# Kernel tuning notes

Measured on AMD Instinct MI355X. Metric: run time of the kernel, lower is better.

Reference implementation:

```python
import jax, jax.numpy as jnp
import numpy as np
import math

ROPE_THETA = 10000.0


def apply_rope(x, positions):
    # x: [B, H, S, d_k], positions: [S]
    d_k = x.shape[-1]
    inv_freq = 1.0 / (ROPE_THETA ** (jnp.arange(0, d_k, 2, dtype=jnp.float32) / d_k))  # [d_k/2]
    angles = positions.astype(jnp.float32)[:, None] * inv_freq[None, :]  # [S, d_k/2]
    cos = jnp.cos(angles)
    sin = jnp.sin(angles)
    x1 = x[..., 0::2]
    x2 = x[..., 1::2]
    r1 = x1 * cos - x2 * sin
    r2 = x1 * sin + x2 * cos
    out = jnp.stack([r1, r2], axis=-1)  # interleave pairs back
    return out.reshape(x.shape)


def setup_inputs() -> dict:
    key = jax.random.key(0)
    k1, k2, k3 = jax.random.split(key, 3)
    B, S, D = 4, 2048, 1024
    x = jax.random.normal(k1, (B, S, D), dtype=jnp.float32)
    token_positions = jnp.arange(S, dtype=jnp.int32)
    w_qkv = jax.random.normal(k2, (3 * D, D), dtype=jnp.float32) * (1.0 / math.sqrt(D))
    w_o = jax.random.normal(k3, (D, D), dtype=jnp.float32) * (1.0 / math.sqrt(D))
    return {"x": x, "token_positions": token_positions, "w_qkv": w_qkv, "w_o": w_o}


def reference(x, token_positions, w_qkv, w_o):
    B, S, D = x.shape
    H = 16
    d_k = D // H
    qkv = jnp.einsum('bsd,ed->bse', x, w_qkv)  # [B, S, 3D]
    # rearrange '... s (stack h dk) -> stack ... h s dk'
    qkv = qkv.reshape(B, S, 3, H, d_k)
    q = jnp.transpose(qkv[:, :, 0], (0, 2, 1, 3))  # [B, H, S, dk]
    k = jnp.transpose(qkv[:, :, 1], (0, 2, 1, 3))
    v = jnp.transpose(qkv[:, :, 2], (0, 2, 1, 3))
    q = apply_rope(q, token_positions)
    k = apply_rope(k, token_positions)
    scores = jnp.einsum('bhqd,bhkd->bhqk', q, k) / math.sqrt(d_k)
    causal = jnp.tril(jnp.ones((S, S), dtype=bool))
    scores = jnp.where(causal[None, None], scores, -jnp.inf)
    attn = jax.nn.softmax(scores, axis=-1)
    out = jnp.einsum('bhqk,bhkd->bhqd', attn, v)  # [B, H, S, dk]
    out = jnp.transpose(out, (0, 2, 1, 3)).reshape(B, S, D)
    return jnp.einsum('bsd,ed->bse', out, w_o)
```

## Files before the change

kernel.cpp:

```cpp
#include <hip/hip_runtime.h>
#include <hip/hip_bf16.h>
#include <math.h>

typedef __bf16 bf16_t;
typedef __attribute__((ext_vector_type(8))) __bf16 bf16x8;
typedef __attribute__((ext_vector_type(4))) __bf16 bf16x4;
typedef __attribute__((ext_vector_type(4))) float f32x4;

#define MFMA_16x16x32(A_, B_, C_) __builtin_amdgcn_mfma_f32_16x16x32_bf16((A_), (B_), (C_), 0, 0, 0)

#define Bsz 4
#define Ssz 2048
#define Dsz 1024
#define Hh 16
#define DKd 64
#define Mrows (Bsz * Ssz)
#define N1 (3 * Dsz)
#define KD Dsz

__global__ void cvt_f32_bf16_kernel(const float* __restrict__ src, bf16_t* __restrict__ dst, int n4) {
  int i = blockIdx.x * blockDim.x + threadIdx.x;
  if (i >= n4) return;
  float4 v = reinterpret_cast<const float4*>(src)[i];
  bf16x4 o = {(bf16_t)v.x, (bf16_t)v.y, (bf16_t)v.z, (bf16_t)v.w};
  reinterpret_cast<bf16x4*>(dst)[i] = o;
}

__global__ void rope_tab_kernel(const int* __restrict__ pos, float2* __restrict__ tab) {
  int i = blockIdx.x * blockDim.x + threadIdx.x;
  if (i >= Ssz * 32) return;
  int s = i >> 5, f = i & 31;
  float inv_freq = powf(10000.0f, -(float)(2 * f) / 64.0f);
  float a = (float)pos[s] * inv_freq;
  tab[i] = make_float2(cosf(a), sinf(a));
}

__global__ __launch_bounds__(512, 1) void gemm256_qkv_kernel(
    const bf16_t* __restrict__ A, const bf16_t* __restrict__ Bt,
    bf16_t* __restrict__ qb, bf16_t* __restrict__ kb, bf16_t* __restrict__ vtb,
    const float2* __restrict__ tab) {
  constexpr int NT = KD / 64;
  __shared__ __align__(16) bf16_t As[2][256 * 64];
  __shared__ __align__(16) bf16_t Bs[2][192 * 64];
  const int t = threadIdx.x;
  const int w = t >> 6, l = t & 63;
  const int lr = l & 15, lk = l >> 4;
  const int rs = lr >> 1;
  const int wm = w >> 2, wn = w & 3;
  const int m0 = blockIdx.y * 256, n0 = blockIdx.x * 192;

  const int gcol = ((t & 7) ^ ((t >> 4) & 7)) * 8;
  const bf16_t* gA = A + (size_t)(m0 + (t >> 3)) * KD + gcol;
  const bf16_t* gB = Bt + (size_t)(n0 + (t >> 3)) * KD + gcol;

  f32x4 acc[8][3] = {};
  bf16x8 bfv[3][2];

#define LDA_(I_, SB_, KT_)                                                        \
  __builtin_amdgcn_global_load_lds(gA + (size_t)(I_) * 64 * KD + (KT_),           \
                                   &As[SB_][((I_) * 64 + w * 8) * 64], 16, 0, 0)
#define LDB_(I_, SB_, KT_)                                                        \
  __builtin_amdgcn_global_load_lds(gB + (size_t)(I_) * 64 * KD + (KT_),           \
                                   &Bs[SB_][((I_) * 64 + w * 8) * 64], 16, 0, 0)

#define PH(BUF_, P_, STG0_, STG1_, VMW_)                                          \
  do {                                                                            \
    if ((P_) == 0) {                                                              \
      _Pragma("unroll") for (int n_ = 0; n_ < 3; ++n_) {                          \
        const int R_ = wn * 48 + n_ * 16 + lr;                                    \
        bfv[n_][0] = *reinterpret_cast<const bf16x8*>(                            \
            &Bs[BUF_][R_ * 64 + ((lk ^ rs) * 8)]);                                \
        bfv[n_][1] = *reinterpret_cast<const bf16x8*>(                            \
            &Bs[BUF_][R_ * 64 + (((4 + lk) ^ rs) * 8)]);                          \
      }                                                                           \
    }                                                                             \
    bf16x8 af0_[2], af1_[2];                                                      \
    {                                                                             \
      const int Ra_ = wm * 128 + (P_) * 32 + lr;                                  \
      const int Rb_ = Ra_ + 16;                                                   \
      af0_[0] = *reinterpret_cast<const bf16x8*>(&As[BUF_][Ra_ * 64 + ((lk ^ rs) * 8)]);       \
      af0_[1] = *reinterpret_cast<const bf16x8*>(&As[BUF_][Ra_ * 64 + (((4 + lk) ^ rs) * 8)]); \
      af1_[0] = *reinterpret_cast<const bf16x8*>(&As[BUF_][Rb_ * 64 + ((lk ^ rs) * 8)]);       \
      af1_[1] = *reinterpret_cast<const bf16x8*>(&As[BUF_][Rb_ * 64 + (((4 + lk) ^ rs) * 8)]); \
    }                                                                             \
    STG0_;                                                                        \
    STG1_;                                                                        \
    __builtin_amdgcn_s_barrier();                                                 \
    asm volatile("s_waitcnt lgkmcnt(0)" ::: "memory");                            \
    __builtin_amdgcn_sched_barrier(0);                                            \
    __builtin_amdgcn_s_setprio(1);                                                \
    _Pragma("unroll") for (int n_ = 0; n_ < 3; ++n_) {                            \
      acc[(P_)*2][n_] = MFMA_16x16x32(af0_[0], bfv[n_][0], acc[(P_)*2][n_]);      \
      acc[(P_)*2][n_] = MFMA_16x16x32(af0_[1], bfv[n_][1], acc[(P_)*2][n_]);      \
      acc[(P_)*2 + 1][n_] = MFMA_16x16x32(af1_[0], bfv[n_][0], acc[(P_)*2 + 1][n_]); \
      acc[(P_)*2 + 1][n_] = MFMA_16x16x32(af1_[1], bfv[n_][1], acc[(P_)*2 + 1][n_]); \
    }                                                                             \
    __builtin_amdgcn_s_setprio(0);                                                \
    VMW_;                                                                         \
    __builtin_amdgcn_s_barrier();                                                 \
  } while (0)

#define VM4_ do { asm volatile("s_waitcnt vmcnt(4)" ::: "memory"); __builtin_amdgcn_sched_barrier(0); } while (0)
#define VM2_ do { asm volatile("s_waitcnt vmcnt(2)" ::: "memory"); __builtin_amdgcn_sched_barrier(0); } while (0)

#define TILE_(BUF_, KTN_)                                                         \
  do {                                                                            \
    PH(BUF_, 0, LDB_(0, (BUF_) ^ 1, KTN_), LDB_(1, (BUF_) ^ 1, KTN_), (void)0);   \
    PH(BUF_, 1, LDB_(2, (BUF_) ^ 1, KTN_), LDA_(0, (BUF_) ^ 1, KTN_), VM4_);      \
    PH(BUF_, 2, LDA_(2, (BUF_) ^ 1, KTN_), LDA_(1, (BUF_) ^ 1, KTN_), (void)0);   \
    PH(BUF_, 3, LDA_(3, (BUF_) ^ 1, KTN_), (void)0, VM2_);                        \
  } while (0)

  LDB_(0, 0, 0); LDB_(1, 0, 0); LDB_(2, 0, 0);
  LDA_(0, 0, 0); LDA_(2, 0, 0); LDA_(1, 0, 0); LDA_(3, 0, 0);
  asm volatile("s_waitcnt vmcnt(2)" ::: "memory");
  __builtin_amdgcn_s_barrier();

#pragma unroll 1
  for (int tt = 0; tt < NT; tt += 2) {
    const int ktn0 = ((tt + 1) & (NT - 1)) * 64;
    TILE_(0, ktn0);
    const int ktn1 = ((tt + 2) & (NT - 1)) * 64;
    TILE_(1, ktn1);
  }
#undef TILE_
#undef VM4_
#undef VM2_
#undef PH
#undef LDA_
#undef LDB_

#pragma unroll
  for (int n = 0; n < 3; ++n) {
    const int colbase = n0 + wn * 48 + n * 16;
    const int sect = colbase >> 10;
    const int h = (colbase >> 6) & 15;
    const int dk = (colbase & 63) + lr;
    if (sect < 2) {
      bf16_t* dst0 = (sect == 0) ? qb : kb;
#pragma unroll
      for (int m = 0; m < 8; ++m)
#pragma unroll
        for (int r = 0; r < 4; ++r) {
          const int grow = m0 + wm * 128 + m * 16 + lk * 4 + r;
          const int bb = grow >> 11, s = grow & (Ssz - 1);
          const float v = acc[m][n][r];
          const float pv = __shfl_xor(v, 1);
          const float2 cs = tab[(s << 5) | (dk >> 1)];
          float vr = (dk & 1) ? (pv * cs.y + v * cs.x) : (v * cs.x - pv * cs.y);
          if (sect == 0) vr *= 0.125f;
          dst0[((size_t)(bb * Hh + h) * Ssz + s) * DKd + dk] = (bf16_t)vr;
        }
    } else {
#pragma unroll
      for (int m = 0; m < 8; ++m) {
        const int grow0 = m0 + wm * 128 + m * 16 + lk * 4;
        const int bb = grow0 >> 11, s0 = grow0 & (Ssz - 1);
        const bf16x4 ov = {(bf16_t)acc[m][n][0], (bf16_t)acc[m][n][1],
                           (bf16_t)acc[m][n][2], (bf16_t)acc[m][n][3]};
        *reinterpret_cast<bf16x4*>(
            vtb + ((size_t)(bb * Hh + h) * DKd + dk) * Ssz + s0) = ov;
      }
    }
  }
}

__global__ __launch_bounds__(512, 1) void gemm_out_kernel(
    const bf16_t* __restrict__ A, const bf16_t* __restrict__ Bt,
    float* __restrict__ fout) {
  constexpr int NT = KD / 64;
  __shared__ __align__(16) bf16_t As[2][256 * 64];
  __shared__ __align__(16) bf16_t Bs[2][128 * 64];
  const int t = threadIdx.x;
  const int w = t >> 6, l = t & 63;
  const int lr = l & 15, lk = l >> 4;
  const int rs = lr >> 1;
  const int wm = w >> 2, wn = w & 3;
  const int m0 = blockIdx.y * 256, n0 = blockIdx.x * 128;

  const int gcol = ((t & 7) ^ ((t >> 4) & 7)) * 8;
  const bf16_t* gA = A + (size_t)(m0 + (t >> 3)) * KD + gcol;
  const bf16_t* gB = Bt + (size_t)(n0 + (t >> 3)) * KD + gcol;

  f32x4 acc[8][2] = {};
  bf16x8 bfv[2][2];

#define OLDA_(I_, SB_, KT_)                                                       \
  __builtin_amdgcn_global_load_lds(gA + (size_t)(I_) * 64 * KD + (KT_),           \
                                   &As[SB_][((I_) * 64 + w * 8) * 64], 16, 0, 0)
#define OLDB_(I_, SB_, KT_)                                                       \
  __builtin_amdgcn_global_load_lds(gB + (size_t)(I_) * 64 * KD + (KT_),           \
                                   &Bs[SB_][((I_) * 64 + w * 8) * 64], 16, 0, 0)

#define OPH(BUF_, P_, STG0_, STG1_, VMW_)                                         \
  do {                                                                            \
    if ((P_) == 0) {                                                              \
      _Pragma("unroll") for (int n_ = 0; n_ < 2; ++n_) {                          \
        const int R_ = wn * 32 + n_ * 16 + lr;                                    \
        bfv[n_][0] = *reinterpret_cast<const bf16x8*>(                            \
            &Bs[BUF_][R_ * 64 + ((lk ^ rs) * 8)]);                                \
        bfv[n_][1] = *reinterpret_cast<const bf16x8*>(                            \
            &Bs[BUF_][R_ * 64 + (((4 + lk) ^ rs) * 8)]);                          \
      }                                                                           \
    }                                                                             \
    bf16x8 af0_[2], af1_[2];                                                      \
    {                                                                             \
      const int Ra_ = wm * 128 + (P_) * 32 + lr;                                  \
      const int Rb_ = Ra_ + 16;                                                   \
      af0_[0] = *reinterpret_cast<const bf16x8*>(&As[BUF_][Ra_ * 64 + ((lk ^ rs) * 8)]);       \
      af0_[1] = *reinterpret_cast<const bf16x8*>(&As[BUF_][Ra_ * 64 + (((4 + lk) ^ rs) * 8)]); \
      af1_[0] = *reinterpret_cast<const bf16x8*>(&As[BUF_][Rb_ * 64 + ((lk ^ rs) * 8)]);       \
      af1_[1] = *reinterpret_cast<const bf16x8*>(&As[BUF_][Rb_ * 64 + (((4 + lk) ^ rs) * 8)]); \
    }                                                                             \
    STG0_;                                                                        \
    STG1_;                                                                        \
    __builtin_amdgcn_s_barrier();                                                 \
    asm volatile("s_waitcnt lgkmcnt(0)" ::: "memory");                            \
    __builtin_amdgcn_sched_barrier(0);                                            \
    __builtin_amdgcn_s_setprio(1);                                                \
    _Pragma("unroll") for (int n_ = 0; n_ < 2; ++n_) {                            \
      acc[(P_)*2][n_] = MFMA_16x16x32(af0_[0], bfv[n_][0], acc[(P_)*2][n_]);      \
      acc[(P_)*2][n_] = MFMA_16x16x32(af0_[1], bfv[n_][1], acc[(P_)*2][n_]);      \
      acc[(P_)*2 + 1][n_] = MFMA_16x16x32(af1_[0], bfv[n_][0], acc[(P_)*2 + 1][n_]); \
      acc[(P_)*2 + 1][n_] = MFMA_16x16x32(af1_[1], bfv[n_][1], acc[(P_)*2 + 1][n_]); \
    }                                                                             \
    __builtin_amdgcn_s_setprio(0);                                                \
    VMW_;                                                                         \
    __builtin_amdgcn_s_barrier();                                                 \
  } while (0)

#define OVM4_ do { asm volatile("s_waitcnt vmcnt(4)" ::: "memory"); __builtin_amdgcn_sched_barrier(0); } while (0)
#define OVM2_ do { asm volatile("s_waitcnt vmcnt(2)" ::: "memory"); __builtin_amdgcn_sched_barrier(0); } while (0)

#define OTILE_(BUF_, KTN_)                                                        \
  do {                                                                            \
    OPH(BUF_, 0, OLDB_(0, (BUF_) ^ 1, KTN_), OLDB_(1, (BUF_) ^ 1, KTN_), (void)0);\
    OPH(BUF_, 1, OLDA_(0, (BUF_) ^ 1, KTN_), OLDA_(2, (BUF_) ^ 1, KTN_), OVM4_);  \
    OPH(BUF_, 2, OLDA_(1, (BUF_) ^ 1, KTN_), OLDA_(3, (BUF_) ^ 1, KTN_), (void)0);\
    OPH(BUF_, 3, (void)0, (void)0, OVM2_);                                        \
  } while (0)

  OLDB_(0, 0, 0); OLDB_(1, 0, 0);
  OLDA_(0, 0, 0); OLDA_(2, 0, 0); OLDA_(1, 0, 0); OLDA_(3, 0, 0);
  asm volatile("s_waitcnt vmcnt(2)" ::: "memory");
  __builtin_amdgcn_s_barrier();

#pragma unroll 1
  for (int tt = 0; tt < NT; tt += 2) {
    const int ktn0 = ((tt + 1) & (NT - 1)) * 64;
    OTILE_(0, ktn0);
    const int ktn1 = ((tt + 2) & (NT - 1)) * 64;
    OTILE_(1, ktn1);
  }
#undef OTILE_
#undef OVM4_
#undef OVM2_
#undef OPH
#undef OLDA_
#undef OLDB_

#pragma unroll
  for (int m = 0; m < 8; ++m)
#pragma unroll
    for (int r = 0; r < 4; ++r) {
      const int grow = m0 + wm * 128 + m * 16 + lk * 4 + r;
      float* op = fout + (size_t)grow * Dsz + n0 + wn * 32 + lr;
      op[0] = acc[m][0][r];
      op[16] = acc[m][1][r];
    }
}

__global__ __launch_bounds__(256, 3) void attn_kernel(
    const bf16_t* __restrict__ qb, const bf16_t* __restrict__ kb,
    const bf16_t* __restrict__ vtb, bf16_t* __restrict__ aout) {
  __shared__ __align__(16) bf16_t Ks[2][64 * 64];
  __shared__ __align__(16) bf16_t Vs[2][64 * 64];
  const int t = threadIdx.x, w = t >> 6, l = t & 63;
  const int lr = l & 15, lk = l >> 4;
  const int bid = blockIdx.x;
  const int bh = (bid & 7) * 8 + ((bid >> 3) & 7);
  const int qt = 15 - (bid >> 6);
  const int q0 = qt * 128;
  const int sub0 = q0 + w * 32;

  const bf16_t* qbase = qb + ((size_t)bh * Ssz + sub0) * DKd;
  bf16x8 qf[2][2];
#pragma unroll
  for (int s = 0; s < 2; ++s) {
    qf[s][0] = *reinterpret_cast<const bf16x8*>(qbase + (s * 16 + lr) * DKd + lk * 8);
    qf[s][1] = *reinterpret_cast<const bf16x8*>(qbase + (s * 16 + lr) * DKd + 32 + lk * 8);
  }

  f32x4 o[2][4] = {};
  float mrow[2] = {-INFINITY, -INFINITY};
  float lsum[2] = {0.f, 0.f};

  const int srow = t >> 2;
  const int scc = (t & 3) * 2;
  const bf16_t* kg = kb + ((size_t)bh * Ssz + srow) * DKd + scc * 8;
  const bf16_t* vg = vtb + ((size_t)bh * DKd + srow) * Ssz + scc * 8;
  const int koff0 = srow * 64 + ((scc ^ (srow & 7)) * 8);
  const int koff1 = srow * 64 + (((scc + 1) ^ (srow & 7)) * 8);
  int voff[4];
#pragma unroll
  for (int u = 0; u < 2; ++u) {
    const int c = scc + u;
    const int B = 32 * (c >> 2) + 16 * (c & 1) + 4 * ((c & 3) >> 1);
    const int ch = B >> 3, off = B & 7;
    voff[2 * u] = srow * 64 + ((ch ^ (srow & 7)) * 8) + off;
    voff[2 * u + 1] = srow * 64 + (((ch + 1) ^ (srow & 7)) * 8) + off;
  }

  const int kvend = q0 + 128;
  bf16x8 pk0 = *reinterpret_cast<const bf16x8*>(kg);
  bf16x8 pk1 = *reinterpret_cast<const bf16x8*>(kg + 8);
  bf16x8 pv0 = *reinterpret_cast<const bf16x8*>(vg);
  bf16x8 pv1 = *reinterpret_cast<const bf16x8*>(vg + 8);

  *reinterpret_cast<bf16x8*>(&Ks[0][koff0]) = pk0;
  *reinterpret_cast<bf16x8*>(&Ks[0][koff1]) = pk1;
  *reinterpret_cast<bf16x4*>(&Vs[0][voff[0]]) = __builtin_shufflevector(pv0, pv0, 0, 1, 2, 3);
  *reinterpret_cast<bf16x4*>(&Vs[0][voff[1]]) = __builtin_shufflevector(pv0, pv0, 4, 5, 6, 7);
  *reinterpret_cast<bf16x4*>(&Vs[0][voff[2]]) = __builtin_shufflevector(pv1, pv1, 0, 1, 2, 3);
  *reinterpret_cast<bf16x4*>(&Vs[0][voff[3]]) = __builtin_shufflevector(pv1, pv1, 4, 5, 6, 7);
  __syncthreads();

  for (int kv = 0; kv < kvend; kv += 64) {
    const int buf = (kv >> 6) & 1;
    const bool more = (kv + 64 < kvend);
    if (more) {
      pk0 = *reinterpret_cast<const bf16x8*>(kg + (size_t)(kv + 64) * DKd);
      pk1 = *reinterpret_cast<const bf16x8*>(kg + (size_t)(kv + 64) * DKd + 8);
      pv0 = *reinterpret_cast<const bf16x8*>(vg + kv + 64);
      pv1 = *reinterpret_cast<const bf16x8*>(vg + kv + 64 + 8);
    }
    const bf16_t* Kb = Ks[buf];
    const bf16_t* Vb = Vs[buf];
#pragma unroll
    for (int s = 0; s < 2; ++s) {
      const int subrow = sub0 + s * 16;
      if (kv > subrow + 15) continue;
      f32x4 sa[4];
#pragma unroll
      for (int n = 0; n < 4; ++n) {
        const int R = n * 16 + lr;
        const bf16x8 a0 = *reinterpret_cast<const bf16x8*>(Kb + R * 64 + ((lk ^ (R & 7)) * 8));
        const bf16x8 a1 = *reinterpret_cast<const bf16x8*>(Kb + R * 64 + (((lk + 4) ^ (R & 7)) * 8));
        f32x4 z = {};
        z = MFMA_16x16x32(a0, qf[s][0], z);
        z = MFMA_16x16x32(a1, qf[s][1], z);
        sa[n] = z;
      }
      if (kv + 63 > subrow) {
        const int qrow = subrow + lr;
        const int kbase = kv + lk * 4;
#pragma unroll
        for (int n = 0; n < 4; ++n)
#pragma unroll
          for (int r = 0; r < 4; ++r)
            if (kbase + n * 16 + r > qrow) sa[n][r] = -INFINITY;
      }
      float mx = fmaxf(fmaxf(fmaxf(sa[0][0], sa[0][1]), fmaxf(sa[0][2], sa[0][3])),
                       fmaxf(fmaxf(sa[1][0], sa[1][1]), fmaxf(sa[1][2], sa[1][3])));
      mx = fmaxf(mx, fmaxf(fmaxf(fmaxf(sa[2][0], sa[2][1]), fmaxf(sa[2][2], sa[2][3])),
                           fmaxf(fmaxf(sa[3][0], sa[3][1]), fmaxf(sa[3][2], sa[3][3]))));
      mx = fmaxf(mx, __shfl_xor(mx, 16));
      mx = fmaxf(mx, __shfl_xor(mx, 32));
      const float mnew = fmaxf(mrow[s], mx);
      const float scl = __expf(mrow[s] - mnew);
      mrow[s] = mnew;
      float ps = 0.f;
#pragma unroll
      for (int n = 0; n < 4; ++n)
#pragma unroll
        for (int r = 0; r < 4; ++r) {
          const float p = __expf(sa[n][r] - mnew);
          sa[n][r] = p;
          ps += p;
        }
      lsum[s] = lsum[s] * scl + ps;
#pragma unroll
      for (int n = 0; n < 4; ++n)
#pragma unroll
        for (int r = 0; r < 4; ++r) o[s][n][r] *= scl;
      bf16x8 pb0, pb1;
#pragma unroll
      for (int r = 0; r < 4; ++r) {
        pb0[r] = (bf16_t)sa[0][r];
        pb0[4 + r] = (bf16_t)sa[1][r];
        pb1[r] = (bf16_t)sa[2][r];
        pb1[4 + r] = (bf16_t)sa[3][r];
      }
#pragma unroll
      for (int n = 0; n < 4; ++n) {
        const int R = n * 16 + lr;
        const bf16x8 v0 = *reinterpret_cast<const bf16x8*>(Vb + R * 64 + ((lk ^ (R & 7)) * 8));
        const bf16x8 v1 = *reinterpret_cast<const bf16x8*>(Vb + R * 64 + (((lk + 4) ^ (R & 7)) * 8));
        o[s][n] = MFMA_16x16x32(v0, pb0, o[s][n]);
        o[s][n] = MFMA_16x16x32(v1, pb1, o[s][n]);
      }
    }
    if (more) {
      bf16_t* Kn = Ks[buf ^ 1];
      bf16_t* Vn = Vs[buf ^ 1];
      *reinterpret_cast<bf16x8*>(&Kn[koff0]) = pk0;
      *reinterpret_cast<bf16x8*>(&Kn[koff1]) = pk1;
      *reinterpret_cast<bf16x4*>(&Vn[voff[0]]) = __builtin_shufflevector(pv0, pv0, 0, 1, 2, 3);
      *reinterpret_cast<bf16x4*>(&Vn[voff[1]]) = __builtin_shufflevector(pv0, pv0, 4, 5, 6, 7);
      *reinterpret_cast<bf16x4*>(&Vn[voff[2]]) = __builtin_shufflevector(pv1, pv1, 0, 1, 2, 3);
      *reinterpret_cast<bf16x4*>(&Vn[voff[3]]) = __builtin_shufflevector(pv1, pv1, 4, 5, 6, 7);
      __syncthreads();
    }
  }
  const int b_ = bh >> 4, h_ = bh & 15;
#pragma unroll
  for (int s = 0; s < 2; ++s) {
    float sm = lsum[s];
    sm += __shfl_xor(sm, 16);
    sm += __shfl_xor(sm, 32);
    const float inv = 1.0f / sm;
    const int qrow = sub0 + s * 16 + lr;
    bf16_t* op = aout + ((size_t)b_ * Ssz + qrow) * Dsz + h_ * DKd + lk * 4;
#pragma unroll
    for (int n = 0; n < 4; ++n) {
      const bf16x4 ov = {(bf16_t)(o[s][n][0] * inv), (bf16_t)(o[s][n][1] * inv),
                         (bf16_t)(o[s][n][2] * inv), (bf16_t)(o[s][n][3] * inv)};
      *reinterpret_cast<bf16x4*>(op + n * 16) = ov;
    }
  }
}

extern "C" void kernel_launch(void* const* d_in, const int* in_sizes, int n_in,
                              void* d_out, int out_size, void* d_ws, size_t ws_size,
                              hipStream_t stream) {
  const float* x = (const float*)d_in[0];
  const int* pos = (const int*)d_in[1];
  const float* wqkv = (const float*)d_in[2];
  const float* wo = (const float*)d_in[3];
  float* out = (float*)d_out;

  bf16_t* xb = (bf16_t*)d_ws;
  bf16_t* wqkvb = xb + (size_t)Mrows * KD;
  bf16_t* wob = wqkvb + (size_t)N1 * KD;
  bf16_t* qbuf = wob + (size_t)Dsz * KD;
  bf16_t* kbuf = qbuf + (size_t)64 * Ssz * DKd;
  bf16_t* vtb = kbuf + (size_t)64 * Ssz * DKd;
  float2* tab = (float2*)(vtb + (size_t)64 * Ssz * DKd);
  bf16_t* aout = xb;

  {
    int n4 = Mrows * KD / 4;
    cvt_f32_bf16_kernel<<<(n4 + 255) / 256, 256, 0, stream>>>(x, xb, n4);
  }
  {
    int n4 = N1 * KD / 4;
    cvt_f32_bf16_kernel<<<(n4 + 255) / 256, 256, 0, stream>>>(wqkv, wqkvb, n4);
  }
  {
    int n4 = Dsz * KD / 4;
    cvt_f32_bf16_kernel<<<(n4 + 255) / 256, 256, 0, stream>>>(wo, wob, n4);
  }
  rope_tab_kernel<<<(Ssz * 32 + 255) / 256, 256, 0, stream>>>(pos, tab);

  gemm256_qkv_kernel<<<dim3(N1 / 192, Mrows / 256), 512, 0, stream>>>(
      xb, wqkvb, qbuf, kbuf, vtb, tab);

  attn_kernel<<<dim3(16 * 64), 256, 0, stream>>>(qbuf, kbuf, vtb, aout);

  gemm_out_kernel<<<dim3(Dsz / 128, Mrows / 256), 512, 0, stream>>>(
      aout, wob, out);
}
```

Before: 178.5 us.

## Merge prep kernels, use exp2 softmax with folded log2e, and lazy rescaling

The three f32-to-bf16 conversion kernels and the RoPE table kernel are merged into one launch to cut launch overhead. The Q scale now folds log2(e) into 1/sqrt(dk), so the attention softmax can use exp2f in place of __expf. The online softmax also skips the running-max update and rescale of the accumulator unless the new block max exceeds the stored max by more than 8 (in log2 units). That saves multiplies per tile, at the cost of values up to 2^8 in the exponent path and bf16 probability precision.

```diff
diff --git a/kernel.cpp b/kernel.cpp
--- a/kernel.cpp
+++ b/kernel.cpp
@@ -18,21 +18,36 @@
 #define N1 (3 * Dsz)
 #define KD Dsz
 
-__global__ void cvt_f32_bf16_kernel(const float* __restrict__ src, bf16_t* __restrict__ dst, int n4) {
-  int i = blockIdx.x * blockDim.x + threadIdx.x;
-  if (i >= n4) return;
-  float4 v = reinterpret_cast<const float4*>(src)[i];
-  bf16x4 o = {(bf16_t)v.x, (bf16_t)v.y, (bf16_t)v.z, (bf16_t)v.w};
-  reinterpret_cast<bf16x4*>(dst)[i] = o;
-}
-
-__global__ void rope_tab_kernel(const int* __restrict__ pos, float2* __restrict__ tab) {
-  int i = blockIdx.x * blockDim.x + threadIdx.x;
-  if (i >= Ssz * 32) return;
-  int s = i >> 5, f = i & 31;
-  float inv_freq = powf(10000.0f, -(float)(2 * f) / 64.0f);
-  float a = (float)pos[s] * inv_freq;
-  tab[i] = make_float2(cosf(a), sinf(a));
+__global__ void prep_kernel(const float* __restrict__ x, const float* __restrict__ wqkv,
+                            const float* __restrict__ wo, const int* __restrict__ pos,
+                            bf16_t* __restrict__ xb, bf16_t* __restrict__ wqkvb,
+                            bf16_t* __restrict__ wob, float2* __restrict__ tab) {
+  constexpr int N4X = Mrows * KD / 4;
+  constexpr int N4W = N1 * KD / 4;
+  constexpr int N4O = Dsz * KD / 4;
+  constexpr int NRT = Ssz * 32;
+  const int i = blockIdx.x * blockDim.x + threadIdx.x;
+  if (i < N4X) {
+    float4 v = reinterpret_cast<const float4*>(x)[i];
+    bf16x4 o = {(bf16_t)v.x, (bf16_t)v.y, (bf16_t)v.z, (bf16_t)v.w};
+    reinterpret_cast<bf16x4*>(xb)[i] = o;
+  } else if (i < N4X + N4W) {
+    const int j = i - N4X;
+    float4 v = reinterpret_cast<const float4*>(wqkv)[j];
+    bf16x4 o = {(bf16_t)v.x, (bf16_t)v.y, (bf16_t)v.z, (bf16_t)v.w};
+    reinterpret_cast<bf16x4*>(wqkvb)[j] = o;
+  } else if (i < N4X + N4W + N4O) {
+    const int j = i - N4X - N4W;
+    float4 v = reinterpret_cast<const float4*>(wo)[j];
+    bf16x4 o = {(bf16_t)v.x, (bf16_t)v.y, (bf16_t)v.z, (bf16_t)v.w};
+    reinterpret_cast<bf16x4*>(wob)[j] = o;
+  } else if (i < N4X + N4W + N4O + NRT) {
+    const int j = i - N4X - N4W - N4O;
+    const int s = j >> 5, f = j & 31;
+    float inv_freq = powf(10000.0f, -(float)(2 * f) / 64.0f);
+    float a = (float)pos[s] * inv_freq;
+    tab[j] = make_float2(cosf(a), sinf(a));
+  }
 }
 
 __global__ __launch_bounds__(512, 1) void gemm256_qkv_kernel(
@@ -148,7 +163,7 @@
           const float pv = __shfl_xor(v, 1);
           const float2 cs = tab[(s << 5) | (dk >> 1)];
           float vr = (dk & 1) ? (pv * cs.y + v * cs.x) : (v * cs.x - pv * cs.y);
-          if (sect == 0) vr *= 0.125f;
+          if (sect == 0) vr *= 0.18033688f;
           dst0[((size_t)(bb * Hh + h) * Ssz + s) * DKd + dk] = (bf16_t)vr;
         }
     } else {
@@ -366,23 +381,26 @@
                            fmaxf(fmaxf(sa[3][0], sa[3][1]), fmaxf(sa[3][2], sa[3][3]))));
       mx = fmaxf(mx, __shfl_xor(mx, 16));
       mx = fmaxf(mx, __shfl_xor(mx, 32));
-      const float mnew = fmaxf(mrow[s], mx);
-      const float scl = __expf(mrow[s] - mnew);
-      mrow[s] = mnew;
+      if (!__all(mx <= mrow[s] + 8.0f)) {
+        const float mnew = fmaxf(mrow[s], mx);
+        const float scl = exp2f(mrow[s] - mnew);
+        mrow[s] = mnew;
+        lsum[s] *= scl;
+#pragma unroll
+        for (int n = 0; n < 4; ++n)
+#pragma unroll
+          for (int r = 0; r < 4; ++r) o[s][n][r] *= scl;
+      }
       float ps = 0.f;
 #pragma unroll
       for (int n = 0; n < 4; ++n)
 #pragma unroll
         for (int r = 0; r < 4; ++r) {
-          const float p = __expf(sa[n][r] - mnew);
+          const float p = exp2f(sa[n][r] - mrow[s]);
           sa[n][r] = p;
           ps += p;
         }
-      lsum[s] = lsum[s] * scl + ps;
-#pragma unroll
-      for (int n = 0; n < 4; ++n)
-#pragma unroll
-        for (int r = 0; r < 4; ++r) o[s][n][r] *= scl;
+      lsum[s] += ps;
       bf16x8 pb0, pb1;
 #pragma unroll
       for (int r = 0; r < 4; ++r) {
@@ -449,18 +467,9 @@
   bf16_t* aout = xb;
 
   {
-    int n4 = Mrows * KD / 4;
-    cvt_f32_bf16_kernel<<<(n4 + 255) / 256, 256, 0, stream>>>(x, xb, n4);
-  }
-  {
-    int n4 = N1 * KD / 4;
-    cvt_f32_bf16_kernel<<<(n4 + 255) / 256, 256, 0, stream>>>(wqkv, wqkvb, n4);
-  }
-  {
-    int n4 = Dsz * KD / 4;
-    cvt_f32_bf16_kernel<<<(n4 + 255) / 256, 256, 0, stream>>>(wo, wob, n4);
-  }
-  rope_tab_kernel<<<(Ssz * 32 + 255) / 256, 256, 0, stream>>>(pos, tab);
+    constexpr int total = Mrows * KD / 4 + N1 * KD / 4 + Dsz * KD / 4 + Ssz * 32;
+    prep_kernel<<<(total + 255) / 256, 256, 0, stream>>>(x, wqkv, wo, pos, xb, wqkvb, wob, tab);
+  }
 
   gemm256_qkv_kernel<<<dim3(N1 / 192, Mrows / 256), 512, 0, stream>>>(
       xb, wqkvb, qbuf, kbuf, vtb, tab);
```

After: 181.1 us. No clear change (+1.5%).
